# Optimization experiments

Measured on AMD Instinct MI355X. Metric: run time of the kernel, lower is better.

The kernel has to match this reference:

```python
import jax, jax.numpy as jnp
import numpy as np

DIM = 2048
N_HEADS = 16
HEAD_DIM = 128
KV_HEADS = 1
ROPE_BASE = 10000.0


def _rope_tables(T, dim, dtype):
    inv_freq = 1.0 / (ROPE_BASE ** (jnp.arange(0, dim, 2, dtype=jnp.float32) / dim))
    t = jnp.arange(T, dtype=jnp.float32)
    freqs = jnp.einsum('i,j->ij', t, inv_freq)          # [T, dim/2]
    emb = jnp.concatenate([freqs, freqs], axis=-1)      # [T, dim]
    cos = jnp.cos(emb)[None, None, :, :].astype(dtype)  # [1,1,T,dim]
    sin = jnp.sin(emb)[None, None, :, :].astype(dtype)
    return cos, sin


def _rotate_half(x):
    x1, x2 = jnp.split(x, 2, axis=-1)
    return jnp.concatenate([-x2, x1], axis=-1)


def setup_inputs() -> dict:
    key = jax.random.key(0)
    k1, k2, k3, k4, k5 = jax.random.split(key, 5)
    B, T = 2, 2048
    x = jax.random.normal(k1, (B, T, DIM), dtype=jnp.float32)
    # additive causal mask: 0 on/below diagonal, -1e9 above
    causal = jnp.triu(jnp.full((T, T), -1e9, dtype=jnp.float32), k=1)
    attn_mask = causal[None, None, :, :]
    s = 1.0 / np.sqrt(DIM)
    wq = jax.random.normal(k2, (DIM, N_HEADS * HEAD_DIM), dtype=jnp.float32) * s
    wk = jax.random.normal(k3, (DIM, KV_HEADS * HEAD_DIM), dtype=jnp.float32) * s
    wv = jax.random.normal(k4, (DIM, KV_HEADS * HEAD_DIM), dtype=jnp.float32) * s
    wo = jax.random.normal(k5, (N_HEADS * HEAD_DIM, DIM), dtype=jnp.float32) * s
    return {"x": x, "attn_mask": attn_mask, "wq": wq, "wk": wk, "wv": wv, "wo": wo}


def reference(x, attn_mask, wq, wk, wv, wo):
    B, T, C = x.shape
    q = (x @ wq).reshape(B, T, N_HEADS, HEAD_DIM).transpose(0, 2, 1, 3)   # [B,H,T,d]
    k = (x @ wk).reshape(B, T, KV_HEADS, HEAD_DIM).transpose(0, 2, 1, 3)  # [B,1,T,d]
    v = (x @ wv).reshape(B, T, KV_HEADS, HEAD_DIM).transpose(0, 2, 1, 3)  # [B,1,T,d]
    cos, sin = _rope_tables(T, HEAD_DIM, x.dtype)
    q = q * cos + _rotate_half(q) * sin
    k = k * cos + _rotate_half(k) * sin
    # KV head broadcasts over the H dim inside matmul (MQA expand path)
    att = jnp.matmul(q, k.swapaxes(-1, -2)) / np.sqrt(HEAD_DIM)          # [B,H,T,T]
    att = att + attn_mask
    w = jax.nn.softmax(att, axis=-1)
    y = jnp.matmul(w, v)                                                  # [B,H,T,d]
    y = y.transpose(0, 2, 1, 3).reshape(B, T, N_HEADS * HEAD_DIM)
    y = y @ wo
    k_exp = jnp.broadcast_to(k, (B, N_HEADS, T, HEAD_DIM))
    v_exp = jnp.broadcast_to(v, (B, N_HEADS, T, HEAD_DIM))
    return y, k_exp, v_exp
```

## Files before the change

### kernel.cpp

```cpp
#include <hip/hip_runtime.h>
#include <hip/hip_bf16.h>
#include <cstdint>
#include <cstddef>

#define B_SZ   2
#define T_SEQ  2048
#define C_DIM  2048
#define NH     16
#define HD     128

typedef __attribute__((ext_vector_type(8))) short s8v;
typedef __attribute__((ext_vector_type(4))) float f32x4;

typedef __attribute__((address_space(3))) char lds_char;
typedef __attribute__((address_space(1))) const char glob_char;

#define QSCALE 0.12751887f

__device__ __forceinline__ unsigned short f2bf(float f) {
    union { float f; uint32_t i; } v; v.f = f;
    uint32_t r = (v.i + 0x7FFFu + ((v.i >> 16) & 1u)) >> 16;
    return (unsigned short)r;
}

__device__ __forceinline__ unsigned short cvt1_bf16(float f) {
    unsigned int w;
    asm("v_cvt_pk_bf16_f32 %0, %1, %2" : "=v"(w) : "v"(f), "v"(f));
    return (unsigned short)w;
}

template <int CTRL>
__device__ __forceinline__ float dpp_ror_f(float x) {
    int t = __builtin_amdgcn_update_dpp(__float_as_int(x), __float_as_int(x),
                                        CTRL, 0xf, 0xf, false);
    return __int_as_float(t);
}
__device__ __forceinline__ float rowmax16(float v) {
    v = fmaxf(v, dpp_ror_f<0x121>(v));
    v = fmaxf(v, dpp_ror_f<0x122>(v));
    v = fmaxf(v, dpp_ror_f<0x124>(v));
    v = fmaxf(v, dpp_ror_f<0x128>(v));
    return v;
}

__global__ void k_f32_to_bf16(const float* __restrict__ in,
                              unsigned short* __restrict__ out, int n4) {
    int i = blockIdx.x * blockDim.x + threadIdx.x;
    int stride = gridDim.x * blockDim.x;
    for (; i < n4; i += stride) {
        float4 v = reinterpret_cast<const float4*>(in)[i];
        ushort4 o;
        o.x = f2bf(v.x); o.y = f2bf(v.y); o.z = f2bf(v.z); o.w = f2bf(v.w);
        reinterpret_cast<ushort4*>(out)[i] = o;
    }
}

__global__ void k_transp_bf16(const float* __restrict__ in,
                              unsigned short* __restrict__ out,
                              int R, int C, int ldo) {
    __shared__ unsigned short tile[64][66];
    int x0 = blockIdx.x * 64, y0 = blockIdx.y * 64;
    int tx = threadIdx.x, ty = threadIdx.y;
#pragma unroll
    for (int j = 0; j < 16; ++j) {
        int r = y0 + ty + j * 4;
        tile[ty + j * 4][tx] = f2bf(in[(size_t)r * C + x0 + tx]);
    }
    __syncthreads();
#pragma unroll
    for (int j = 0; j < 16; ++j) {
        int orow = x0 + ty + j * 4;
        out[(size_t)orow * ldo + y0 + tx] = tile[tx][ty + j * 4];
    }
}

__global__ void k_rope_tab(float* __restrict__ cosT, float* __restrict__ sinT,
                           float* __restrict__ cosT2, float* __restrict__ sinT2) {
    int idx = blockIdx.x * blockDim.x + threadIdx.x;
    if (idx >= T_SEQ * 64) return;
    int t = idx >> 6, i = idx & 63;
    float inv = powf(10000.0f, -(float)i / 64.0f);
    float ang = (float)t * inv;
    float c = cosf(ang), s = sinf(ang);
    cosT[idx] = c;  sinT[idx] = s;
    cosT2[i * T_SEQ + t] = c;  sinT2[i * T_SEQ + t] = s;
}

#define BM 128
#define BN 128
#define BK 64

__global__ __launch_bounds__(256) void k_gemm_bt(
        const unsigned short* __restrict__ A,
        const unsigned short* __restrict__ Bt,
        float* __restrict__ C, int M, int N, int K, int ldc, int gx) {
    __shared__ char smem[BM * BK * 2 + BN * BK * 2];
    char* As = smem;
    char* Bs = smem + BM * BK * 2;
    int tid = threadIdx.x, lane = tid & 63, wid = tid >> 6;
    int nwg = gridDim.x, cpx = nwg >> 3;
    int orig = blockIdx.x;
    int wg = (orig & 7) * cpx + (orig >> 3);
    int bx = wg % gx, by = wg / gx;
    int m0 = by * BM, n0 = bx * BN;
    int wr = wid >> 1, wc = wid & 1;

    f32x4 acc[4][4] = {};

    int srow = wid * 32 + (lane >> 3);
    int cp = lane & 7;

    for (int k0 = 0; k0 < K; k0 += BK) {
#pragma unroll
        for (int i = 0; i < 4; ++i) {
            int row = srow + i * 8;
            int c = cp ^ (row & 7);
            const unsigned short* ga = A + (size_t)(m0 + row) * K + k0 + c * 8;
            const unsigned short* gb = Bt + (size_t)(n0 + row) * K + k0 + c * 8;
            __builtin_amdgcn_global_load_lds((glob_char*)ga,
                (lds_char*)(As + wid * 4096 + i * 1024), 16, 0, 0);
            __builtin_amdgcn_global_load_lds((glob_char*)gb,
                (lds_char*)(Bs + wid * 4096 + i * 1024), 16, 0, 0);
        }
        __syncthreads();

#pragma unroll
        for (int kc = 0; kc < 2; ++kc) {
            s8v af[4], bfr[4];
#pragma unroll
            for (int mi = 0; mi < 4; ++mi) {
                int row = wr * 64 + mi * 16 + (lane & 15);
                int slot = (kc * 4 + (lane >> 4)) ^ (row & 7);
                af[mi] = *reinterpret_cast<const s8v*>(As + row * 128 + slot * 16);
            }
#pragma unroll
            for (int ni = 0; ni < 4; ++ni) {
                int row = wc * 64 + ni * 16 + (lane & 15);
                int slot = (kc * 4 + (lane >> 4)) ^ (row & 7);
                bfr[ni] = *reinterpret_cast<const s8v*>(Bs + row * 128 + slot * 16);
            }
#pragma unroll
            for (int mi = 0; mi < 4; ++mi)
#pragma unroll
                for (int ni = 0; ni < 4; ++ni)
                    acc[mi][ni] = __builtin_amdgcn_mfma_f32_16x16x32_bf16(
                        af[mi], bfr[ni], acc[mi][ni], 0, 0, 0);
        }
        __syncthreads();
    }

#pragma unroll
    for (int mi = 0; mi < 4; ++mi) {
        int row = m0 + wr * 64 + mi * 16 + ((lane >> 4) << 2);
#pragma unroll
        for (int ni = 0; ni < 4; ++ni) {
            int col = n0 + wc * 64 + ni * 16 + (lane & 15);
            float* cp2 = C + (size_t)row * ldc + col;
#pragma unroll
            for (int r = 0; r < 4; ++r)
                cp2[(size_t)r * ldc] = acc[mi][ni][r];
        }
    }
}

__global__ __launch_bounds__(256) void k_gemm_qkv(
        const unsigned short* __restrict__ A,
        const unsigned short* __restrict__ Bt,
        const float* __restrict__ cosT2,
        const float* __restrict__ sinT2,
        unsigned short* __restrict__ qB,
        float* __restrict__ qkvKV) {
    const int GX = 18, K = 2048;
    __shared__ char smem[BM * BK * 2 + BN * BK * 2];
    char* As = smem;
    char* Bs = smem + BM * BK * 2;
    int tid = threadIdx.x, lane = tid & 63, wid = tid >> 6;
    int nwg = gridDim.x, cpx = nwg >> 3;
    int orig = blockIdx.x;
    int wg = (orig & 7) * cpx + (orig >> 3);
    int bx = wg % GX, by = wg / GX;
    int m0 = by * BM, n0 = bx * BN;
    int l15 = lane & 15, l4 = lane >> 4;

    f32x4 acc[2][8] = {};

    int srow = wid * 32 + (lane >> 3);
    int cp = lane & 7;

    for (int k0 = 0; k0 < K; k0 += BK) {
#pragma unroll
        for (int i = 0; i < 4; ++i) {
            int row = srow + i * 8;
            int c = cp ^ (row & 7);
            const unsigned short* ga = A + (size_t)(m0 + row) * K + k0 + c * 8;
            const unsigned short* gb = Bt + (size_t)(n0 + row) * K + k0 + c * 8;
            __builtin_amdgcn_global_load_lds((glob_char*)ga,
                (lds_char*)(As + wid * 4096 + i * 1024), 16, 0, 0);
            __builtin_amdgcn_global_load_lds((glob_char*)gb,
                (lds_char*)(Bs + wid * 4096 + i * 1024), 16, 0, 0);
        }
        __syncthreads();

#pragma unroll
        for (int kc = 0; kc < 2; ++kc) {
            s8v af[2], bfr[8];
#pragma unroll
            for (int mi = 0; mi < 2; ++mi) {
                int row = wid * 32 + mi * 16 + l15;
                int slot = (kc * 4 + l4) ^ (row & 7);
                af[mi] = *reinterpret_cast<const s8v*>(As + row * 128 + slot * 16);
            }
#pragma unroll
            for (int ni = 0; ni < 8; ++ni) {
                int row = ni * 16 + l15;
                int slot = (kc * 4 + l4) ^ (row & 7);
                bfr[ni] = *reinterpret_cast<const s8v*>(Bs + row * 128 + slot * 16);
            }
#pragma unroll
            for (int mi = 0; mi < 2; ++mi)
#pragma unroll
                for (int ni = 0; ni < 8; ++ni)
                    acc[mi][ni] = __builtin_amdgcn_mfma_f32_16x16x32_bf16(
                        af[mi], bfr[ni], acc[mi][ni], 0, 0, 0);
        }
        __syncthreads();
    }

    if (bx < 16) {
        int b = m0 >> 11, h = bx;
#pragma unroll
        for (int mi = 0; mi < 2; ++mi) {
            int t0 = (m0 + wid * 32 + mi * 16 + l4 * 4) & (T_SEQ - 1);
#pragma unroll
            for (int nip = 0; nip < 4; ++nip) {
                int d = nip * 16 + l15;
                float4 c4 = *reinterpret_cast<const float4*>(cosT2 + (size_t)d * T_SEQ + t0);
                float4 s4 = *reinterpret_cast<const float4*>(sinT2 + (size_t)d * T_SEQ + t0);
#pragma unroll
                for (int r = 0; r < 4; ++r) {
                    float x1 = acc[mi][nip][r];
                    float x2 = acc[mi][nip + 4][r];
                    float cc = (&c4.x)[r], ss = (&s4.x)[r];
                    float o1 = (x1 * cc - x2 * ss) * QSCALE;
                    float o2 = (x2 * cc + x1 * ss) * QSCALE;
                    size_t qoff = ((size_t)(b * NH + h) * T_SEQ + t0 + r) * HD + d;
                    qB[qoff] = cvt1_bf16(o1);
                    qB[qoff + 64] = cvt1_bf16(o2);
                }
            }
        }
    } else {
        int colb = (bx - 16) * 128;
#pragma unroll
        for (int mi = 0; mi < 2; ++mi) {
            int row = m0 + wid * 32 + mi * 16 + l4 * 4;
#pragma unroll
            for (int ni = 0; ni < 8; ++ni) {
                int col = colb + ni * 16 + l15;
                float* cp2 = qkvKV + (size_t)row * 256 + col;
#pragma unroll
                for (int r = 0; r < 4; ++r)
                    cp2[(size_t)r * 256] = acc[mi][ni][r];
            }
        }
    }
}

__global__ void k_kv_transform(const float* __restrict__ qkvKV,
                               const float* __restrict__ cosT,
                               const float* __restrict__ sinT,
                               unsigned short* __restrict__ kB,
                               unsigned short* __restrict__ vT,
                               float* __restrict__ kexp,
                               float* __restrict__ vexp) {
    int bt = blockIdx.x;
    int b = bt >> 11, t = bt & 2047;
    int tid = threadIdx.x;
    const float* base = qkvKV + (size_t)bt * 256;

    if (tid < 64) {
        int d = tid;
        float c = cosT[t * 64 + d], s = sinT[t * 64 + d];
        float k1 = base[d], k2 = base[d + 64];
        float o1 = k1 * c - k2 * s;
        float o2 = k2 * c + k1 * s;
        size_t koff = ((size_t)b * T_SEQ + t) * HD + d;
        kB[koff] = f2bf(o1);
        kB[koff + 64] = f2bf(o2);
#pragma unroll
        for (int h = 0; h < NH; ++h) {
            size_t eoff = ((size_t)(b * NH + h) * T_SEQ + t) * HD + d;
            kexp[eoff] = o1;
            kexp[eoff + 64] = o2;
        }
    }
    if (tid >= 128) {
        int d = tid - 128;
        float v = base[128 + d];
        vT[((size_t)b * HD + d) * T_SEQ + t] = f2bf(v);
#pragma unroll
        for (int h = 0; h < NH; ++h)
            vexp[((size_t)(b * NH + h) * T_SEQ + t) * HD + d] = v;
    }
}

__global__ __launch_bounds__(256, 2) void k_flash_attn(
        const unsigned short* __restrict__ qB,
        const unsigned short* __restrict__ kB,
        const unsigned short* __restrict__ vT,
        unsigned short* __restrict__ yattn) {
    __shared__ char smem[81920];
    int tid = threadIdx.x, lane = tid & 63, wvid = tid >> 6;
    int blk = blockIdx.x;
    int b = blk >> 8;
    int rem = blk & 255;
    int h = rem & 15;
    int jj = rem >> 4;
    int j0 = 16 + jj;
    int j1 = 15 - jj;
    int qrow0[2];
    qrow0[0] = j0 * 64 + wvid * 16;
    qrow0[1] = j1 * 64 + wvid * 16;

    char* Ks0 = smem;
    char* Vs0 = smem + 32768;
    char* pbase = smem + 65536 + wvid * 4096;

    const unsigned short* kbB   = kB + (size_t)b * T_SEQ * HD;
    const unsigned short* vbase = vT + (size_t)b * HD * T_SEQ;

    s8v aq[2][4];
#pragma unroll
    for (int rt = 0; rt < 2; ++rt) {
        const unsigned short* qbase =
            qB + ((size_t)(b * NH + h) * T_SEQ + qrow0[rt]) * HD;
#pragma unroll
        for (int kc = 0; kc < 4; ++kc)
            aq[rt][kc] = *reinterpret_cast<const s8v*>(
                qbase + (size_t)(lane & 15) * HD + kc * 32 + (lane >> 4) * 8);
    }

    float m_r[2][4], l_r[2][4];
#pragma unroll
    for (int rt = 0; rt < 2; ++rt)
#pragma unroll
        for (int r = 0; r < 4; ++r) { m_r[rt][r] = -3e38f; l_r[rt][r] = 0.f; }
    f32x4 o[2][8] = {};

    int NT = j0 + 1;

    auto stage = [&](int buf, int t) {
        int kv0 = t * 64;
#pragma unroll
        for (int j = 0; j < 4; ++j) {
            int n = j * 256 + tid;
            int row = n >> 4, ch = n & 15;
            const unsigned short* src =
                kbB + (size_t)(kv0 + row) * HD + (ch ^ (row & 7)) * 8;
            __builtin_amdgcn_global_load_lds((glob_char*)src,
                (lds_char*)(Ks0 + buf * 16384 + j * 4096 + wvid * 1024), 16, 0, 0);
        }
#pragma unroll
        for (int j = 0; j < 4; ++j) {
            int n = j * 256 + tid;
            int row = n >> 3, ch = n & 7;
            const unsigned short* src =
                vbase + (size_t)row * T_SEQ + kv0 + (ch ^ (row & 7)) * 8;
            __builtin_amdgcn_global_load_lds((glob_char*)src,
                (lds_char*)(Vs0 + buf * 16384 + j * 4096 + wvid * 1024), 16, 0, 0);
        }
    };

    stage(0, 0);
    asm volatile("s_waitcnt vmcnt(0)" ::: "memory");
    __builtin_amdgcn_s_barrier();
    __builtin_amdgcn_sched_barrier(0);

    for (int t = 0; t < NT; ++t) {
        int cur = t & 1;
        if (t + 1 < NT) stage(cur ^ 1, t + 1);
        int kv0 = t * 64;
        const char* Kc = Ks0 + cur * 16384;
        const char* Vc = Vs0 + cur * 16384;
        int act1 = (t <= j1);

        f32x4 sfr[2][4] = {};
        __builtin_amdgcn_s_setprio(1);
#pragma unroll
        for (int kc = 0; kc < 4; ++kc) {
            s8v kf[4];
#pragma unroll
            for (int n = 0; n < 4; ++n) {
                int row = n * 16 + (lane & 15);
                int byte = row * 256 +
                    ((kc * 64 + (lane >> 4) * 16) ^ ((row & 7) << 4));
                kf[n] = *reinterpret_cast<const s8v*>(Kc + byte);
            }
#pragma unroll
            for (int n = 0; n < 4; ++n)
                sfr[0][n] = __builtin_amdgcn_mfma_f32_16x16x32_bf16(
                    aq[0][kc], kf[n], sfr[0][n], 0, 0, 0);
            if (act1) {
#pragma unroll
                for (int n = 0; n < 4; ++n)
                    sfr[1][n] = __builtin_amdgcn_mfma_f32_16x16x32_bf16(
                        aq[1][kc], kf[n], sfr[1][n], 0, 0, 0);
            }
        }
        __builtin_amdgcn_s_setprio(0);

#pragma unroll
        for (int rt = 0; rt < 2; ++rt) {
            if (rt == 1 && !act1) continue;
            if (kv0 + 63 > qrow0[rt]) {
#pragma unroll
                for (int n = 0; n < 4; ++n)
#pragma unroll
                    for (int r = 0; r < 4; ++r) {
                        int col = kv0 + n * 16 + (lane & 15);
                        int row = qrow0[rt] + ((lane >> 4) << 2) + r;
                        if (col > row) sfr[rt][n][r] = -1e9f;
                    }
            }
            float pm[4];
#pragma unroll
            for (int r = 0; r < 4; ++r) {
                float v0 = fmaxf(fmaxf(sfr[rt][0][r], sfr[rt][1][r]),
                                 fmaxf(sfr[rt][2][r], sfr[rt][3][r]));
                pm[r] = rowmax16(v0);
            }
            int ok = (pm[0] <= m_r[rt][0] + 8.0f) &
                     (pm[1] <= m_r[rt][1] + 8.0f) &
                     (pm[2] <= m_r[rt][2] + 8.0f) &
                     (pm[3] <= m_r[rt][3] + 8.0f);
            if (!__all(ok)) {
#pragma unroll
                for (int r = 0; r < 4; ++r) {
                    float mn = fmaxf(m_r[rt][r], pm[r]);
                    float al = exp2f(m_r[rt][r] - mn);
                    l_r[rt][r] *= al;
#pragma unroll
                    for (int ds = 0; ds < 8; ++ds)
                        o[rt][ds][r] *= al;
                    m_r[rt][r] = mn;
                }
            }
#pragma unroll
            for (int n = 0; n < 4; ++n)
#pragma unroll
                for (int r = 0; r < 4; ++r) {
                    float p = exp2f(sfr[rt][n][r] - m_r[rt][r]);
                    sfr[rt][n][r] = p;
                    l_r[rt][r] += p;
                }
        }

#pragma unroll
        for (int rt = 0; rt < 2; ++rt) {
            if (rt == 1 && !act1) continue;
#pragma unroll
            for (int n = 0; n < 4; ++n)
#pragma unroll
                for (int r = 0; r < 4; ++r) {
                    int rowl = rt * 16 + ((lane >> 4) << 2) + r;
                    int byte = rowl * 128 + (n * 16 + (lane & 15)) * 2;
                    byte ^= ((rowl & 7) << 4);
                    *reinterpret_cast<unsigned short*>(pbase + byte) =
                        cvt1_bf16(sfr[rt][n][r]);
                }
        }
        asm volatile("s_waitcnt lgkmcnt(0)" ::: "memory");
        __builtin_amdgcn_sched_barrier(0);

        __builtin_amdgcn_s_setprio(1);
#pragma unroll
        for (int kc2 = 0; kc2 < 2; ++kc2) {
            s8v pa[2];
#pragma unroll
            for (int rt = 0; rt < 2; ++rt) {
                int rowl = rt * 16 + (lane & 15);
                int byte = rowl * 128 +
                    ((kc2 * 64 + (lane >> 4) * 16) ^ ((rowl & 7) << 4));
                pa[rt] = *reinterpret_cast<const s8v*>(pbase + byte);
            }
#pragma unroll
            for (int ds = 0; ds < 8; ++ds) {
                int vrow = ds * 16 + (lane & 15);
                int vbyte = vrow * 128 +
                    ((kc2 * 64 + (lane >> 4) * 16) ^ ((vrow & 7) << 4));
                s8v bv = *reinterpret_cast<const s8v*>(Vc + vbyte);
                o[0][ds] = __builtin_amdgcn_mfma_f32_16x16x32_bf16(
                    pa[0], bv, o[0][ds], 0, 0, 0);
                if (act1)
                    o[1][ds] = __builtin_amdgcn_mfma_f32_16x16x32_bf16(
                        pa[1], bv, o[1][ds], 0, 0, 0);
            }
        }
        __builtin_amdgcn_s_setprio(0);

        asm volatile("s_waitcnt vmcnt(0) lgkmcnt(0)" ::: "memory");
        __builtin_amdgcn_s_barrier();
        __builtin_amdgcn_sched_barrier(0);
    }

#pragma unroll
    for (int rt = 0; rt < 2; ++rt) {
        float inv[4];
#pragma unroll
        for (int r = 0; r < 4; ++r) {
            float lv = l_r[rt][r];
#pragma unroll
            for (int off = 1; off < 16; off <<= 1)
                lv += __shfl_xor(lv, off);
            inv[r] = 1.0f / lv;
        }
#pragma unroll
        for (int ds = 0; ds < 8; ++ds)
#pragma unroll
            for (int r = 0; r < 4; ++r) {
                int row = qrow0[rt] + ((lane >> 4) << 2) + r;
                int col = h * HD + ds * 16 + (lane & 15);
                yattn[((size_t)b * T_SEQ + row) * C_DIM + col] =
                    cvt1_bf16(o[rt][ds][r] * inv[r]);
            }
    }
}

extern "C" void kernel_launch(void* const* d_in, const int* in_sizes, int n_in,
                              void* d_out, int out_size, void* d_ws, size_t ws_size,
                              hipStream_t stream) {
    const float* x  = (const float*)d_in[0];
    const float* wq = (const float*)d_in[2];
    const float* wk = (const float*)d_in[3];
    const float* wv = (const float*)d_in[4];
    const float* wo = (const float*)d_in[5];

    char* ws = (char*)d_ws;
    size_t off = 0;
    auto alloc = [&](size_t bytes) -> void* {
        void* p = ws + off;
        off += (bytes + 255) & ~(size_t)255;
        return p;
    };
    unsigned short* xb    = (unsigned short*)alloc((size_t)4096 * 2048 * 2);
    unsigned short* wT    = (unsigned short*)alloc((size_t)2304 * 2048 * 2);
    unsigned short* woT   = (unsigned short*)alloc((size_t)2048 * 2048 * 2);
    float*          qkvKV = (float*)alloc((size_t)4096 * 256 * 4);
    float*          cosT  = (float*)alloc((size_t)2048 * 64 * 4);
    float*          sinT  = (float*)alloc((size_t)2048 * 64 * 4);
    float*          cosT2 = (float*)alloc((size_t)64 * 2048 * 4);
    float*          sinT2 = (float*)alloc((size_t)64 * 2048 * 4);
    unsigned short* qB    = (unsigned short*)alloc((size_t)2 * 16 * 2048 * 128 * 2);
    unsigned short* kB    = (unsigned short*)alloc((size_t)2 * 2048 * 128 * 2);
    unsigned short* vT    = (unsigned short*)alloc((size_t)2 * 128 * 2048 * 2);
    unsigned short* yattn = (unsigned short*)alloc((size_t)4096 * 2048 * 2);

    float* y_out = (float*)d_out;
    float* kexp  = y_out + (size_t)2 * 2048 * 2048;
    float* vexp  = kexp + (size_t)2 * 16 * 2048 * 128;

    dim3 tb(64, 4);
    k_f32_to_bf16<<<2048, 256, 0, stream>>>(x, xb, 4096 * 2048 / 4);
    k_transp_bf16<<<dim3(32, 32), tb, 0, stream>>>(wq, wT, 2048, 2048, 2048);
    k_transp_bf16<<<dim3(2, 32), tb, 0, stream>>>(wk, wT + (size_t)2048 * 2048, 2048, 128, 2048);
    k_transp_bf16<<<dim3(2, 32), tb, 0, stream>>>(wv, wT + (size_t)2176 * 2048, 2048, 128, 2048);
    k_transp_bf16<<<dim3(32, 32), tb, 0, stream>>>(wo, woT, 2048, 2048, 2048);
    k_rope_tab<<<512, 256, 0, stream>>>(cosT, sinT, cosT2, sinT2);

    k_gemm_qkv<<<576, 256, 0, stream>>>(xb, wT, cosT2, sinT2, qB, qkvKV);
    k_kv_transform<<<4096, 256, 0, stream>>>(qkvKV, cosT, sinT, kB, vT, kexp, vexp);
    k_flash_attn<<<512, 256, 0, stream>>>(qB, kB, vT, yattn);
    k_gemm_bt<<<512, 256, 0, stream>>>(
        yattn, woT, y_out, 4096, 2048, 2048, 2048, 16);
}
```

Baseline: 249.1 us.

## Halve flash-attention KV tile to 32 and raise occupancy to four blocks

The flash attention kernel now processes 32-key tiles instead of 64, halving shared memory (80KB to 40KB) so launch bounds can request 4 blocks per CU instead of 2. Causal skipping becomes per-wave and per-row-tile at 32-key granularity, so less masked work is computed, and the K, V and P swizzle patterns are adjusted for the narrower tiles. The cost is twice as many iterations, each with its own barrier and softmax rescale, plus a tighter register budget that may cause spills given the accumulator arrays.

```diff
diff --git a/kernel.cpp b/kernel.cpp
--- a/kernel.cpp
+++ b/kernel.cpp
@@ -304,13 +304,14 @@
     }
 }
 
-__global__ __launch_bounds__(256, 2) void k_flash_attn(
+__global__ __launch_bounds__(256, 4) void k_flash_attn(
         const unsigned short* __restrict__ qB,
         const unsigned short* __restrict__ kB,
         const unsigned short* __restrict__ vT,
         unsigned short* __restrict__ yattn) {
-    __shared__ char smem[81920];
+    __shared__ char smem[40960];
     int tid = threadIdx.x, lane = tid & 63, wvid = tid >> 6;
+    int l15 = lane & 15, l4 = lane >> 4;
     int blk = blockIdx.x;
     int b = blk >> 8;
     int rem = blk & 255;
@@ -323,8 +324,8 @@
     qrow0[1] = j1 * 64 + wvid * 16;
 
     char* Ks0 = smem;
-    char* Vs0 = smem + 32768;
-    char* pbase = smem + 65536 + wvid * 4096;
+    char* Vs0 = smem + 16384;
+    char* pbase = smem + 32768 + wvid * 2048;
 
     const unsigned short* kbB   = kB + (size_t)b * T_SEQ * HD;
     const unsigned short* vbase = vT + (size_t)b * HD * T_SEQ;
@@ -337,7 +338,7 @@
 #pragma unroll
         for (int kc = 0; kc < 4; ++kc)
             aq[rt][kc] = *reinterpret_cast<const s8v*>(
-                qbase + (size_t)(lane & 15) * HD + kc * 32 + (lane >> 4) * 8);
+                qbase + (size_t)l15 * HD + kc * 32 + l4 * 8);
     }
 
     float m_r[2][4], l_r[2][4];
@@ -347,27 +348,27 @@
         for (int r = 0; r < 4; ++r) { m_r[rt][r] = -3e38f; l_r[rt][r] = 0.f; }
     f32x4 o[2][8] = {};
 
-    int NT = j0 + 1;
+    int NT = 2 * j0 + 2;
 
     auto stage = [&](int buf, int t) {
-        int kv0 = t * 64;
-#pragma unroll
-        for (int j = 0; j < 4; ++j) {
+        int kv0 = t * 32;
+#pragma unroll
+        for (int j = 0; j < 2; ++j) {
             int n = j * 256 + tid;
             int row = n >> 4, ch = n & 15;
             const unsigned short* src =
                 kbB + (size_t)(kv0 + row) * HD + (ch ^ (row & 7)) * 8;
             __builtin_amdgcn_global_load_lds((glob_char*)src,
-                (lds_char*)(Ks0 + buf * 16384 + j * 4096 + wvid * 1024), 16, 0, 0);
-        }
-#pragma unroll
-        for (int j = 0; j < 4; ++j) {
+                (lds_char*)(Ks0 + buf * 8192 + j * 4096 + wvid * 1024), 16, 0, 0);
+        }
+#pragma unroll
+        for (int j = 0; j < 2; ++j) {
             int n = j * 256 + tid;
-            int row = n >> 3, ch = n & 7;
+            int row = n >> 2, ch = n & 3;
             const unsigned short* src =
-                vbase + (size_t)row * T_SEQ + kv0 + (ch ^ (row & 7)) * 8;
+                vbase + (size_t)row * T_SEQ + kv0 + (ch ^ ((row >> 1) & 3)) * 8;
             __builtin_amdgcn_global_load_lds((glob_char*)src,
-                (lds_char*)(Vs0 + buf * 16384 + j * 4096 + wvid * 1024), 16, 0, 0);
+                (lds_char*)(Vs0 + buf * 8192 + j * 4096 + wvid * 1024), 16, 0, 0);
         }
     };
 
@@ -379,30 +380,33 @@
     for (int t = 0; t < NT; ++t) {
         int cur = t & 1;
         if (t + 1 < NT) stage(cur ^ 1, t + 1);
-        int kv0 = t * 64;
-        const char* Kc = Ks0 + cur * 16384;
-        const char* Vc = Vs0 + cur * 16384;
-        int act1 = (t <= j1);
-
-        f32x4 sfr[2][4] = {};
+        int kv0 = t * 32;
+        const char* Kc = Ks0 + cur * 8192;
+        const char* Vc = Vs0 + cur * 8192;
+        int act[2];
+        act[0] = (kv0 <= qrow0[0] + 15);
+        act[1] = (kv0 <= qrow0[1] + 15);
+
+        f32x4 sfr[2][2] = {};
         __builtin_amdgcn_s_setprio(1);
 #pragma unroll
         for (int kc = 0; kc < 4; ++kc) {
-            s8v kf[4];
-#pragma unroll
-            for (int n = 0; n < 4; ++n) {
-                int row = n * 16 + (lane & 15);
-                int byte = row * 256 +
-                    ((kc * 64 + (lane >> 4) * 16) ^ ((row & 7) << 4));
+            s8v kf[2];
+#pragma unroll
+            for (int n = 0; n < 2; ++n) {
+                int row = n * 16 + l15;
+                int byte = row * 256 + ((kc * 64 + l4 * 16) ^ ((row & 7) << 4));
                 kf[n] = *reinterpret_cast<const s8v*>(Kc + byte);
             }
-#pragma unroll
-            for (int n = 0; n < 4; ++n)
-                sfr[0][n] = __builtin_amdgcn_mfma_f32_16x16x32_bf16(
-                    aq[0][kc], kf[n], sfr[0][n], 0, 0, 0);
-            if (act1) {
-#pragma unroll
-                for (int n = 0; n < 4; ++n)
+            if (act[0]) {
+#pragma unroll
+                for (int n = 0; n < 2; ++n)
+                    sfr[0][n] = __builtin_amdgcn_mfma_f32_16x16x32_bf16(
+                        aq[0][kc], kf[n], sfr[0][n], 0, 0, 0);
+            }
+            if (act[1]) {
+#pragma unroll
+                for (int n = 0; n < 2; ++n)
                     sfr[1][n] = __builtin_amdgcn_mfma_f32_16x16x32_bf16(
                         aq[1][kc], kf[n], sfr[1][n], 0, 0, 0);
             }
@@ -411,22 +415,21 @@
 
 #pragma unroll
         for (int rt = 0; rt < 2; ++rt) {
-            if (rt == 1 && !act1) continue;
-            if (kv0 + 63 > qrow0[rt]) {
-#pragma unroll
-                for (int n = 0; n < 4; ++n)
+            if (!act[rt]) continue;
+            if (kv0 + 31 > qrow0[rt]) {
+#pragma unroll
+                for (int n = 0; n < 2; ++n)
 #pragma unroll
                     for (int r = 0; r < 4; ++r) {
-                        int col = kv0 + n * 16 + (lane & 15);
-                        int row = qrow0[rt] + ((lane >> 4) << 2) + r;
+                        int col = kv0 + n * 16 + l15;
+                        int row = qrow0[rt] + (l4 << 2) + r;
                         if (col > row) sfr[rt][n][r] = -1e9f;
                     }
             }
             float pm[4];
 #pragma unroll
             for (int r = 0; r < 4; ++r) {
-                float v0 = fmaxf(fmaxf(sfr[rt][0][r], sfr[rt][1][r]),
-                                 fmaxf(sfr[rt][2][r], sfr[rt][3][r]));
+                float v0 = fmaxf(sfr[rt][0][r], sfr[rt][1][r]);
                 pm[r] = rowmax16(v0);
             }
             int ok = (pm[0] <= m_r[rt][0] + 8.0f) &
@@ -446,7 +449,7 @@
                 }
             }
 #pragma unroll
-            for (int n = 0; n < 4; ++n)
+            for (int n = 0; n < 2; ++n)
 #pragma unroll
                 for (int r = 0; r < 4; ++r) {
                     float p = exp2f(sfr[rt][n][r] - m_r[rt][r]);
@@ -457,14 +460,14 @@
 
 #pragma unroll
         for (int rt = 0; rt < 2; ++rt) {
-            if (rt == 1 && !act1) continue;
-#pragma unroll
-            for (int n = 0; n < 4; ++n)
+            if (!act[rt]) continue;
+#pragma unroll
+            for (int n = 0; n < 2; ++n)
 #pragma unroll
                 for (int r = 0; r < 4; ++r) {
-                    int rowl = rt * 16 + ((lane >> 4) << 2) + r;
-                    int byte = rowl * 128 + (n * 16 + (lane & 15)) * 2;
-                    byte ^= ((rowl & 7) << 4);
+                    int rowl = rt * 16 + (l4 << 2) + r;
+                    int byte = rowl * 64 +
+                        (((n * 16 + l15) * 2) ^ (((rowl >> 2) & 3) << 4));
                     *reinterpret_cast<unsigned short*>(pbase + byte) =
                         cvt1_bf16(sfr[rt][n][r]);
                 }
@@ -473,25 +476,23 @@
         __builtin_amdgcn_sched_barrier(0);
 
         __builtin_amdgcn_s_setprio(1);
-#pragma unroll
-        for (int kc2 = 0; kc2 < 2; ++kc2) {
+        {
             s8v pa[2];
 #pragma unroll
             for (int rt = 0; rt < 2; ++rt) {
-                int rowl = rt * 16 + (lane & 15);
-                int byte = rowl * 128 +
-                    ((kc2 * 64 + (lane >> 4) * 16) ^ ((rowl & 7) << 4));
+                int rowl = rt * 16 + l15;
+                int byte = rowl * 64 + ((l4 * 16) ^ (((rowl >> 2) & 3) << 4));
                 pa[rt] = *reinterpret_cast<const s8v*>(pbase + byte);
             }
 #pragma unroll
             for (int ds = 0; ds < 8; ++ds) {
-                int vrow = ds * 16 + (lane & 15);
-                int vbyte = vrow * 128 +
-                    ((kc2 * 64 + (lane >> 4) * 16) ^ ((vrow & 7) << 4));
+                int vrow = ds * 16 + l15;
+                int vbyte = vrow * 64 + ((l4 * 16) ^ (((vrow >> 1) & 3) << 4));
                 s8v bv = *reinterpret_cast<const s8v*>(Vc + vbyte);
-                o[0][ds] = __builtin_amdgcn_mfma_f32_16x16x32_bf16(
-                    pa[0], bv, o[0][ds], 0, 0, 0);
-                if (act1)
+                if (act[0])
+                    o[0][ds] = __builtin_amdgcn_mfma_f32_16x16x32_bf16(
+                        pa[0], bv, o[0][ds], 0, 0, 0);
+                if (act[1])
                     o[1][ds] = __builtin_amdgcn_mfma_f32_16x16x32_bf16(
                         pa[1], bv, o[1][ds], 0, 0, 0);
             }
@@ -518,8 +519,8 @@
         for (int ds = 0; ds < 8; ++ds)
 #pragma unroll
             for (int r = 0; r < 4; ++r) {
-                int row = qrow0[rt] + ((lane >> 4) << 2) + r;
-                int col = h * HD + ds * 16 + (lane & 15);
+                int row = qrow0[rt] + (l4 << 2) + r;
+                int col = h * HD + ds * 16 + l15;
                 yattn[((size_t)b * T_SEQ + row) * C_DIM + col] =
                     cvt1_bf16(o[rt][ds][r] * inv[r]);
             }
```

After: 362.5 us. +45.5%, slower.
